# Kernel optimization log

Measured on AMD Instinct MI355X. Metric: run time of the kernel, lower is better.

Reference implementation:

```python
import jax, jax.numpy as jnp
import numpy as np

TRUNCATE = 4.0
SIGMA_MIN, SIGMA_MAX, NUM_STEPS = 0.5, 20.0, 200
RADIUS = int(TRUNCATE * SIGMA_MAX + 0.5)  # 80
KSIZE = 2 * RADIUS + 1                    # 161
B, C, H, W = 64, 3, 512, 512


def setup_inputs() -> dict:
    key = jax.random.key(0)
    k1, k2 = jax.random.split(key)
    x = jax.random.normal(k1, (B, C, H, W), dtype=jnp.float32)
    # geometric sigma schedule, as used in inverse-heat-dissipation models
    blur_sigmas = jnp.exp(
        jnp.linspace(np.log(SIGMA_MIN), np.log(SIGMA_MAX), NUM_STEPS)
    ).astype(jnp.float32)
    fwd_steps = jax.random.randint(k2, (B,), 0, NUM_STEPS, dtype=jnp.int32)
    return {"x": x, "blur_sigmas": blur_sigmas, "fwd_steps": fwd_steps}


def _gaussian_kernels_1d(sigmas, dtype):
    # torchvision formula: normalized exp(-0.5*(t/sigma)^2) on linspace(-half, half, K)
    half = (KSIZE - 1) / 2.0
    t = jnp.linspace(-half, half, KSIZE, dtype=dtype)        # [K]
    pdf = jnp.exp(-0.5 * (t[None, :] / sigmas[:, None]) ** 2)  # [B, K]
    return pdf / pdf.sum(axis=1, keepdims=True)


def reference(x, blur_sigmas, fwd_steps):
    b, c, h, w = x.shape
    sig = blur_sigmas[fwd_steps] + 1e-6                      # [B] per-sample sigma
    k1d = _gaussian_kernels_1d(sig, x.dtype)                 # [B, K]
    kc = jnp.repeat(k1d, c, axis=0)                          # [B*C, K] depthwise

    pad = KSIZE // 2
    xp = jnp.pad(x, ((0, 0), (0, 0), (pad, pad), (pad, pad)), mode="reflect")
    lhs = xp.reshape(1, b * c, h + 2 * pad, w + 2 * pad)

    dn_shape = (1, b * c, 1, 1)  # placeholder rhs shape for dim numbers
    dn = jax.lax.conv_dimension_numbers(lhs.shape, (b * c, 1, KSIZE, 1),
                                        ("NCHW", "OIHW", "NCHW"))
    # vertical pass: [1, BC, H+2p, W+2p] -> [1, BC, H, W+2p]
    y = jax.lax.conv_general_dilated(
        lhs, kc.reshape(b * c, 1, KSIZE, 1), (1, 1), "VALID",
        dimension_numbers=dn, feature_group_count=b * c)
    # horizontal pass: -> [1, BC, H, W]
    y = jax.lax.conv_general_dilated(
        y, kc.reshape(b * c, 1, 1, KSIZE), (1, 1), "VALID",
        dimension_numbers=dn, feature_group_count=b * c)
    return y.reshape(b, c, h, w)
```

## Files before the change

### kernel.cpp

```cpp
#include <hip/hip_runtime.h>
#include <hip/hip_fp16.h>


#define B_   64
#define C_   3
#define H_   512
#define W_   512
#define RMAX 80
#define NW   224
#define WOFF 112
#define RROW 288
#define SROW 64

typedef float    f32x16 __attribute__((ext_vector_type(16)));
typedef _Float16 f16x8  __attribute__((ext_vector_type(8)));

__device__ __forceinline__ int refl(int g) {
    int a = g < 0 ? -g : g;
    int c = 1022 - a;
    return a < c ? a : c;
}

__global__ __launch_bounds__(256) void k_weights(const float* __restrict__ sig,
                                                 const int* __restrict__ steps,
                                                 int* __restrict__ rad,
                                                 unsigned int* __restrict__ gw2) {
    const int b = blockIdx.x;
    const float sigma = sig[steps[b]] + 1e-6f;
    const int t = (int)threadIdx.x;
    const int d = t - 128;
    float e = 0.f;
    if (d >= -RMAX && d <= RMAX) {
        const float u = (float)d / sigma;
        e = expf(-0.5f * u * u);
    }
    __shared__ float red[256];
    __shared__ float wv[256];
    red[t] = e;
    __syncthreads();
    for (int s = 128; s > 0; s >>= 1) {
        if (t < s) red[t] += red[t + s];
        __syncthreads();
    }
    const float inv = 1.0f / red[0];
    int r = (int)ceilf(6.0f * sigma);
    if (r > RMAX) r = RMAX;
    if (r < 1)    r = 1;
    wv[t] = (d >= -r && d <= r) ? e * inv : 0.f;
    __syncthreads();
    if (t < NW) {
        const __half h0 = __float2half(wv[t + 16]);
        const __half h1 = __float2half(wv[t + 17]);
        gw2[b * NW + t] = (unsigned int)__half_as_ushort(h0) |
                          ((unsigned int)__half_as_ushort(h1) << 16);
    }
    if (t == 0) rad[b] = r;
}

__global__ __launch_bounds__(256, 4) void k_pass1(const float* __restrict__ x,
                                                  const unsigned int* __restrict__ gw2,
                                                  const int* __restrict__ rad,
                                                  __half* __restrict__ tmp) {
    __shared__ __align__(16) unsigned short sh[SROW * RROW];
    __shared__ unsigned int w2v[NW];
    const int tid = threadIdx.x;
    const int bid = blockIdx.x;
    const int bc  = bid >> 5;
    const int rem = bid & 31;
    const int y0  = (rem >> 3) << 7;
    const int x0  = (rem & 7) << 6;
    const int b   = bc / C_;
    const size_t img = (size_t)bc * (H_ * (size_t)W_);

    const int r  = rad[b];
    const int rp = (r + 7) & ~7;
    const int ns = (r + rp + 32 + 15) >> 4;
    const int Rr = 96 + 16 * ns;
    const int ystart = y0 - rp;

    if (tid < NW) w2v[tid] = gw2[b * NW + tid];

    {
        const int p0 = tid & 15;
        const int x4 = tid >> 4;
        const float* gsrc = x + img + (size_t)(x0 + x4 * 4);
        const int i7 = (2 * p0) & 7;
        for (int pr = p0; 2 * pr < Rr; pr += 16) {
            const int i0 = 2 * pr;
            const int gy0 = refl(ystart + i0);
            const int gy1 = refl(ystart + i0 + 1);
            const float4 va = *(const float4*)(gsrc + (size_t)gy0 * W_);
            const float4 vb = *(const float4*)(gsrc + (size_t)gy1 * W_);
            const int c = i0 >> 3;
            #pragma unroll
            for (int q = 0; q < 4; ++q) {
                const int xq = x4 * 4 + q;
                const int hidx = xq * RROW + ((c ^ (xq & 3)) << 3) + i7;
                const float fa = q == 0 ? va.x : q == 1 ? va.y : q == 2 ? va.z : va.w;
                const float fb = q == 0 ? vb.x : q == 1 ? vb.y : q == 2 ? vb.z : vb.w;
                *(__half2*)(sh + hidx) = __floats2half2_rn(fa, fb);
            }
        }
    }
    __syncthreads();

    const int l   = tid & 63;
    const int tau = tid >> 6;
    const int m   = l & 31;
    const int g   = l >> 5;
    const int ebase = WOFF + 8 * g - rp - m;
    const int cb0 = 4 * tau + g;
    const int key = m & 3;
    const int bb0 = m * RROW;
    const int bb1 = (32 + m) * RROW;

    f32x16 acc0 = {};
    f32x16 acc1 = {};
    for (int s = 0; s < ns; ++s) {
        const int e = ebase + 16 * s;
        union { unsigned int u[4]; f16x8 h; } A;
        A.u[0] = w2v[e];     A.u[1] = w2v[e + 2];
        A.u[2] = w2v[e + 4]; A.u[3] = w2v[e + 6];
        const int ph = ((cb0 + 2 * s) ^ key) << 3;
        const f16x8 bf0 = *(const f16x8*)(sh + bb0 + ph);
        const f16x8 bf1 = *(const f16x8*)(sh + bb1 + ph);
        acc0 = __builtin_amdgcn_mfma_f32_32x32x16_f16(A.h, bf0, acc0, 0, 0, 0);
        acc1 = __builtin_amdgcn_mfma_f32_32x32x16_f16(A.h, bf1, acc1, 0, 0, 0);
    }

    __half* tb = tmp + img + (size_t)(y0 + 32 * tau) * W_ + x0 + m;
    #pragma unroll
    for (int reg = 0; reg < 16; ++reg) {
        const int row = (reg & 3) + 8 * (reg >> 2) + 4 * g;
        tb[(size_t)row * W_]      = __float2half(acc0[reg]);
        tb[(size_t)row * W_ + 32] = __float2half(acc1[reg]);
    }
}

__global__ __launch_bounds__(256, 4) void k_pass2(const __half* __restrict__ tmp,
                                                  const unsigned int* __restrict__ gw2,
                                                  const int* __restrict__ rad,
                                                  float* __restrict__ out) {
    __shared__ __align__(16) unsigned short sh[SROW * RROW];
    __shared__ unsigned int w2v[NW];
    const int tid = threadIdx.x;
    const int bid = blockIdx.x;
    const int bc  = bid >> 5;
    const int rem = bid & 31;
    const int y0  = (rem >> 2) << 6;
    const int x0  = (rem & 3) << 7;
    const int b   = bc / C_;
    const size_t img = (size_t)bc * (H_ * (size_t)W_);

    const int r   = rad[b];
    const int rp  = (r + 7) & ~7;
    const int ns  = (r + rp + 32 + 15) >> 4;
    const int NC  = 12 + 2 * ns;
    const int i0g = x0 - rp;

    if (tid < NW) w2v[tid] = gw2[b * NW + tid];

    {
        const int row  = tid >> 2;
        const int cq   = tid & 3;
        const __half* grow = tmp + img + (size_t)(y0 + row) * W_;
        const int rkey = row & 3;
        for (int c = cq; c < NC; c += 4) {
            const int gi = i0g + c * 8;
            const int hidx = row * RROW + ((c ^ rkey) << 3);
            if (gi >= 0 && gi + 8 <= W_) {
                *(int4*)(sh + hidx) = *(const int4*)(grow + gi);
            } else {
                #pragma unroll
                for (int j = 0; j < 8; ++j)
                    sh[hidx + j] = __half_as_ushort(grow[refl(gi + j)]);
            }
        }
    }
    __syncthreads();

    const int l   = tid & 63;
    const int w   = tid >> 6;
    const int m   = l & 31;
    const int g   = l >> 5;
    const int tau = w >> 1;
    const int nup = (w & 1) * 2;
    const int ebase = WOFF + 8 * g - rp - m;
    const int arow  = 32 * tau + m;
    const int abase = arow * RROW;
    const int akey  = arow & 3;
    const int ca0   = 4 * nup + g;

    f32x16 acc0 = {};
    f32x16 acc1 = {};
    for (int s = 0; s < ns; ++s) {
        const int e = ebase + 16 * s;
        union { unsigned int u[4]; f16x8 h; } Wf;
        Wf.u[0] = w2v[e];     Wf.u[1] = w2v[e + 2];
        Wf.u[2] = w2v[e + 4]; Wf.u[3] = w2v[e + 6];
        const int c = ca0 + 2 * s;
        const f16x8 af0 = *(const f16x8*)(sh + abase + ((c ^ akey) << 3));
        const f16x8 af1 = *(const f16x8*)(sh + abase + (((c + 4) ^ akey) << 3));
        acc0 = __builtin_amdgcn_mfma_f32_32x32x16_f16(af0, Wf.h, acc0, 0, 0, 0);
        acc1 = __builtin_amdgcn_mfma_f32_32x32x16_f16(af1, Wf.h, acc1, 0, 0, 0);
    }

    float* ob = out + img + (size_t)(y0 + 32 * tau) * W_ + x0 + 32 * nup + m;
    #pragma unroll
    for (int reg = 0; reg < 16; ++reg) {
        const int row = (reg & 3) + 8 * (reg >> 2) + 4 * g;
        ob[(size_t)row * W_]      = acc0[reg];
        ob[(size_t)row * W_ + 32] = acc1[reg];
    }
}

extern "C" void kernel_launch(void* const* d_in, const int* in_sizes, int n_in,
                              void* d_out, int out_size, void* d_ws, size_t ws_size,
                              hipStream_t stream) {
    const float* x     = (const float*)d_in[0];
    const float* sig   = (const float*)d_in[1];
    const int*   steps = (const int*)d_in[2];
    float* out = (float*)d_out;

    char* ws = (char*)d_ws;
    int*          rad = (int*)ws;
    unsigned int* gw2 = (unsigned int*)(ws + 1024);
    __half*       tmp = (__half*)(ws + 65536);

    k_weights<<<B_, 256, 0, stream>>>(sig, steps, rad, gw2);
    k_pass1<<<B_ * C_ * 32, 256, 0, stream>>>(x, gw2, rad, tmp);
    k_pass2<<<B_ * C_ * 32, 256, 0, stream>>>(tmp, gw2, rad, out);
}
```

Before: 420.1 us.

## Fuse weight generation into passes and enlarge tiles for more halo reuse

Removes the separate weight kernel: each block of both passes now builds the Gaussian weights itself in shared memory. Pass 1 tiles grow to 256 rows by 64 columns with four accumulators per wave, and the block index is remapped so blocks of the same image run close together. Pass 2 now loads full 512-wide rows and fills the reflected halo inside shared memory instead of branching on global loads. The aim is to cut halo re-reads and one launch. The cost is redundant weight computation per block, more shared memory and fewer blocks, which may reduce occupancy.

New measurement: 398.3 us. 5.2% less time.

```diff
diff --git a/kernel.cpp b/kernel.cpp
--- a/kernel.cpp
+++ b/kernel.cpp
@@ -9,8 +9,8 @@
 #define RMAX 80
 #define NW   224
 #define WOFF 112
-#define RROW 288
-#define SROW 64
+#define RROW1 416
+#define IW2   672
 
 typedef float    f32x16 __attribute__((ext_vector_type(16)));
 typedef _Float16 f16x8  __attribute__((ext_vector_type(8)));
@@ -21,64 +21,59 @@
     return a < c ? a : c;
 }
 
-__global__ __launch_bounds__(256) void k_weights(const float* __restrict__ sig,
-                                                 const int* __restrict__ steps,
-                                                 int* __restrict__ rad,
-                                                 unsigned int* __restrict__ gw2) {
-    const int b = blockIdx.x;
-    const float sigma = sig[steps[b]] + 1e-6f;
-    const int t = (int)threadIdx.x;
-    const int d = t - 128;
+__device__ __forceinline__ int make_weights(float sigma, float* scr, float* red,
+                                            unsigned int* w2v, int tid) {
+    const int d = tid - 128;
     float e = 0.f;
     if (d >= -RMAX && d <= RMAX) {
         const float u = (float)d / sigma;
         e = expf(-0.5f * u * u);
     }
-    __shared__ float red[256];
-    __shared__ float wv[256];
-    red[t] = e;
+    scr[tid] = e;
+    red[tid] = e;
     __syncthreads();
     for (int s = 128; s > 0; s >>= 1) {
-        if (t < s) red[t] += red[t + s];
+        if (tid < s) red[tid] += red[tid + s];
         __syncthreads();
     }
     const float inv = 1.0f / red[0];
     int r = (int)ceilf(6.0f * sigma);
     if (r > RMAX) r = RMAX;
     if (r < 1)    r = 1;
-    wv[t] = (d >= -r && d <= r) ? e * inv : 0.f;
-    __syncthreads();
-    if (t < NW) {
-        const __half h0 = __float2half(wv[t + 16]);
-        const __half h1 = __float2half(wv[t + 17]);
-        gw2[b * NW + t] = (unsigned int)__half_as_ushort(h0) |
-                          ((unsigned int)__half_as_ushort(h1) << 16);
-    }
-    if (t == 0) rad[b] = r;
-}
-
-__global__ __launch_bounds__(256, 4) void k_pass1(const float* __restrict__ x,
-                                                  const unsigned int* __restrict__ gw2,
-                                                  const int* __restrict__ rad,
-                                                  __half* __restrict__ tmp) {
-    __shared__ __align__(16) unsigned short sh[SROW * RROW];
+    if (tid < NW) {
+        const int d0 = tid - 112;
+        const float w0 = (d0     >= -r && d0     <= r) ? scr[tid + 16] * inv : 0.f;
+        const float w1 = (d0 + 1 >= -r && d0 + 1 <= r) ? scr[tid + 17] * inv : 0.f;
+        w2v[tid] = (unsigned int)__half_as_ushort(__float2half(w0)) |
+                   ((unsigned int)__half_as_ushort(__float2half(w1)) << 16);
+    }
+    __syncthreads();
+    return r;
+}
+
+__global__ __launch_bounds__(256) void k_pass1(const float* __restrict__ x,
+                                               const float* __restrict__ sig,
+                                               const int* __restrict__ steps,
+                                               __half* __restrict__ tmp) {
+    __shared__ __align__(16) unsigned short sh[64 * RROW1];
     __shared__ unsigned int w2v[NW];
     const int tid = threadIdx.x;
-    const int bid = blockIdx.x;
-    const int bc  = bid >> 5;
-    const int rem = bid & 31;
-    const int y0  = (rem >> 3) << 7;
+    int bid = blockIdx.x;
+    bid = ((bid & 7) * 384) + (bid >> 3);
+    const int bc  = bid >> 4;
+    const int rem = bid & 15;
+    const int y0  = (rem >> 3) << 8;
     const int x0  = (rem & 7) << 6;
     const int b   = bc / C_;
     const size_t img = (size_t)bc * (H_ * (size_t)W_);
 
-    const int r  = rad[b];
+    const float sigma = sig[steps[b]] + 1e-6f;
+    float* scr = (float*)sh;
+    const int r  = make_weights(sigma, scr, scr + 256, w2v, tid);
     const int rp = (r + 7) & ~7;
-    const int ns = (r + rp + 32 + 15) >> 4;
-    const int Rr = 96 + 16 * ns;
+    const int ns = (r + rp + 47) >> 4;
+    const int Rr = 224 + 16 * ns;
     const int ystart = y0 - rp;
-
-    if (tid < NW) w2v[tid] = gw2[b * NW + tid];
 
     {
         const int p0 = tid & 15;
@@ -86,131 +81,146 @@
         const float* gsrc = x + img + (size_t)(x0 + x4 * 4);
         const int i7 = (2 * p0) & 7;
         for (int pr = p0; 2 * pr < Rr; pr += 16) {
-            const int i0 = 2 * pr;
+            const int i0  = 2 * pr;
             const int gy0 = refl(ystart + i0);
             const int gy1 = refl(ystart + i0 + 1);
             const float4 va = *(const float4*)(gsrc + (size_t)gy0 * W_);
             const float4 vb = *(const float4*)(gsrc + (size_t)gy1 * W_);
+            const float* fa = (const float*)&va;
+            const float* fb = (const float*)&vb;
             const int c = i0 >> 3;
             #pragma unroll
             for (int q = 0; q < 4; ++q) {
                 const int xq = x4 * 4 + q;
-                const int hidx = xq * RROW + ((c ^ (xq & 3)) << 3) + i7;
-                const float fa = q == 0 ? va.x : q == 1 ? va.y : q == 2 ? va.z : va.w;
-                const float fb = q == 0 ? vb.x : q == 1 ? vb.y : q == 2 ? vb.z : vb.w;
-                *(__half2*)(sh + hidx) = __floats2half2_rn(fa, fb);
+                const int hidx = xq * RROW1 + ((c ^ (xq & 3)) << 3) + i7;
+                *(__half2*)(sh + hidx) = __floats2half2_rn(fa[q], fb[q]);
             }
         }
     }
     __syncthreads();
 
     const int l   = tid & 63;
-    const int tau = tid >> 6;
+    const int wv_ = tid >> 6;
     const int m   = l & 31;
     const int g   = l >> 5;
+    const int key = m & 3;
     const int ebase = WOFF + 8 * g - rp - m;
-    const int cb0 = 4 * tau + g;
-    const int key = m & 3;
-    const int bb0 = m * RROW;
-    const int bb1 = (32 + m) * RROW;
-
-    f32x16 acc0 = {};
-    f32x16 acc1 = {};
+    const int cA  = 4 * wv_ + g;
+    const int cB  = 4 * (wv_ + 4) + g;
+    const unsigned short* shm0 = sh + m * RROW1;
+    const unsigned short* shm1 = sh + (32 + m) * RROW1;
+
+    f32x16 a0 = {}, a1 = {}, a2 = {}, a3 = {};
     for (int s = 0; s < ns; ++s) {
         const int e = ebase + 16 * s;
         union { unsigned int u[4]; f16x8 h; } A;
         A.u[0] = w2v[e];     A.u[1] = w2v[e + 2];
         A.u[2] = w2v[e + 4]; A.u[3] = w2v[e + 6];
-        const int ph = ((cb0 + 2 * s) ^ key) << 3;
-        const f16x8 bf0 = *(const f16x8*)(sh + bb0 + ph);
-        const f16x8 bf1 = *(const f16x8*)(sh + bb1 + ph);
-        acc0 = __builtin_amdgcn_mfma_f32_32x32x16_f16(A.h, bf0, acc0, 0, 0, 0);
-        acc1 = __builtin_amdgcn_mfma_f32_32x32x16_f16(A.h, bf1, acc1, 0, 0, 0);
-    }
-
-    __half* tb = tmp + img + (size_t)(y0 + 32 * tau) * W_ + x0 + m;
+        const int phA = ((cA + 2 * s) ^ key) << 3;
+        const int phB = ((cB + 2 * s) ^ key) << 3;
+        const f16x8 b00 = *(const f16x8*)(shm0 + phA);
+        const f16x8 b01 = *(const f16x8*)(shm1 + phA);
+        const f16x8 b10 = *(const f16x8*)(shm0 + phB);
+        const f16x8 b11 = *(const f16x8*)(shm1 + phB);
+        a0 = __builtin_amdgcn_mfma_f32_32x32x16_f16(A.h, b00, a0, 0, 0, 0);
+        a1 = __builtin_amdgcn_mfma_f32_32x32x16_f16(A.h, b01, a1, 0, 0, 0);
+        a2 = __builtin_amdgcn_mfma_f32_32x32x16_f16(A.h, b10, a2, 0, 0, 0);
+        a3 = __builtin_amdgcn_mfma_f32_32x32x16_f16(A.h, b11, a3, 0, 0, 0);
+    }
+
+    __half* tb0 = tmp + img + (size_t)(y0 + 32 * wv_) * W_ + x0 + m;
+    __half* tb1 = tmp + img + (size_t)(y0 + 32 * (wv_ + 4)) * W_ + x0 + m;
     #pragma unroll
     for (int reg = 0; reg < 16; ++reg) {
         const int row = (reg & 3) + 8 * (reg >> 2) + 4 * g;
-        tb[(size_t)row * W_]      = __float2half(acc0[reg]);
-        tb[(size_t)row * W_ + 32] = __float2half(acc1[reg]);
-    }
-}
-
-__global__ __launch_bounds__(256, 4) void k_pass2(const __half* __restrict__ tmp,
-                                                  const unsigned int* __restrict__ gw2,
-                                                  const int* __restrict__ rad,
-                                                  float* __restrict__ out) {
-    __shared__ __align__(16) unsigned short sh[SROW * RROW];
+        tb0[(size_t)row * W_]      = __float2half(a0[reg]);
+        tb0[(size_t)row * W_ + 32] = __float2half(a1[reg]);
+        tb1[(size_t)row * W_]      = __float2half(a2[reg]);
+        tb1[(size_t)row * W_ + 32] = __float2half(a3[reg]);
+    }
+}
+
+__global__ __launch_bounds__(256) void k_pass2(const __half* __restrict__ tmp,
+                                               const float* __restrict__ sig,
+                                               const int* __restrict__ steps,
+                                               float* __restrict__ out) {
+    __shared__ __align__(16) unsigned short sh[32 * IW2];
     __shared__ unsigned int w2v[NW];
     const int tid = threadIdx.x;
     const int bid = blockIdx.x;
-    const int bc  = bid >> 5;
-    const int rem = bid & 31;
-    const int y0  = (rem >> 2) << 6;
-    const int x0  = (rem & 3) << 7;
+    const int bc  = bid >> 4;
+    const int y0  = (bid & 15) << 5;
     const int b   = bc / C_;
     const size_t img = (size_t)bc * (H_ * (size_t)W_);
 
-    const int r   = rad[b];
-    const int rp  = (r + 7) & ~7;
-    const int ns  = (r + rp + 32 + 15) >> 4;
-    const int NC  = 12 + 2 * ns;
-    const int i0g = x0 - rp;
-
-    if (tid < NW) w2v[tid] = gw2[b * NW + tid];
-
+    const float sigma = sig[steps[b]] + 1e-6f;
+    float* scr = (float*)sh;
+    const int r  = make_weights(sigma, scr, scr + 256, w2v, tid);
+    const int rp = (r + 7) & ~7;
+    const int ns = (r + rp + 47) >> 4;
+
+    const int row  = tid >> 3;
+    const int cq   = tid & 7;
+    const int rkey = row & 3;
     {
-        const int row  = tid >> 2;
-        const int cq   = tid & 3;
         const __half* grow = tmp + img + (size_t)(y0 + row) * W_;
-        const int rkey = row & 3;
-        for (int c = cq; c < NC; c += 4) {
-            const int gi = i0g + c * 8;
-            const int hidx = row * RROW + ((c ^ rkey) << 3);
-            if (gi >= 0 && gi + 8 <= W_) {
-                *(int4*)(sh + hidx) = *(const int4*)(grow + gi);
-            } else {
-                #pragma unroll
-                for (int j = 0; j < 8; ++j)
-                    sh[hidx + j] = __half_as_ushort(grow[refl(gi + j)]);
-            }
+        const int cb = rp >> 3;
+        for (int k = cq; k < 64; k += 8) {
+            const int c = cb + k;
+            *(int4*)(sh + row * IW2 + ((c ^ rkey) << 3)) =
+                *(const int4*)(grow + k * 8);
         }
     }
     __syncthreads();
+    {
+        const int nh = 16 * ns - 32;
+        const int rbase = row * IW2;
+        for (int e = cq; e < nh; e += 8) {
+            const int ip = e < rp ? e : e + 512;
+            const int gx = ip - rp;
+            const int is = refl(gx) + rp;
+            const unsigned short v =
+                sh[rbase + (((is >> 3) ^ rkey) << 3) + (is & 7)];
+            sh[rbase + (((ip >> 3) ^ rkey) << 3) + (ip & 7)] = v;
+        }
+    }
+    __syncthreads();
 
     const int l   = tid & 63;
-    const int w   = tid >> 6;
+    const int wv_ = tid >> 6;
     const int m   = l & 31;
     const int g   = l >> 5;
-    const int tau = w >> 1;
-    const int nup = (w & 1) * 2;
+    const int akey  = m & 3;
     const int ebase = WOFF + 8 * g - rp - m;
-    const int arow  = 32 * tau + m;
-    const int abase = arow * RROW;
-    const int akey  = arow & 3;
-    const int ca0   = 4 * nup + g;
-
-    f32x16 acc0 = {};
-    f32x16 acc1 = {};
+    const unsigned short* shm = sh + m * IW2;
+    const int c0 = 16 * wv_ + g;
+
+    f32x16 a0 = {}, a1 = {}, a2 = {}, a3 = {};
     for (int s = 0; s < ns; ++s) {
         const int e = ebase + 16 * s;
         union { unsigned int u[4]; f16x8 h; } Wf;
         Wf.u[0] = w2v[e];     Wf.u[1] = w2v[e + 2];
         Wf.u[2] = w2v[e + 4]; Wf.u[3] = w2v[e + 6];
-        const int c = ca0 + 2 * s;
-        const f16x8 af0 = *(const f16x8*)(sh + abase + ((c ^ akey) << 3));
-        const f16x8 af1 = *(const f16x8*)(sh + abase + (((c + 4) ^ akey) << 3));
-        acc0 = __builtin_amdgcn_mfma_f32_32x32x16_f16(af0, Wf.h, acc0, 0, 0, 0);
-        acc1 = __builtin_amdgcn_mfma_f32_32x32x16_f16(af1, Wf.h, acc1, 0, 0, 0);
-    }
-
-    float* ob = out + img + (size_t)(y0 + 32 * tau) * W_ + x0 + 32 * nup + m;
+        const int cs = c0 + 2 * s;
+        const f16x8 f0 = *(const f16x8*)(shm + (((cs     ) ^ akey) << 3));
+        const f16x8 f1 = *(const f16x8*)(shm + (((cs +  4) ^ akey) << 3));
+        const f16x8 f2 = *(const f16x8*)(shm + (((cs +  8) ^ akey) << 3));
+        const f16x8 f3 = *(const f16x8*)(shm + (((cs + 12) ^ akey) << 3));
+        a0 = __builtin_amdgcn_mfma_f32_32x32x16_f16(f0, Wf.h, a0, 0, 0, 0);
+        a1 = __builtin_amdgcn_mfma_f32_32x32x16_f16(f1, Wf.h, a1, 0, 0, 0);
+        a2 = __builtin_amdgcn_mfma_f32_32x32x16_f16(f2, Wf.h, a2, 0, 0, 0);
+        a3 = __builtin_amdgcn_mfma_f32_32x32x16_f16(f3, Wf.h, a3, 0, 0, 0);
+    }
+
+    float* ob = out + img + (size_t)y0 * W_ + 128 * wv_ + m;
     #pragma unroll
     for (int reg = 0; reg < 16; ++reg) {
-        const int row = (reg & 3) + 8 * (reg >> 2) + 4 * g;
-        ob[(size_t)row * W_]      = acc0[reg];
-        ob[(size_t)row * W_ + 32] = acc1[reg];
+        const int orow = (reg & 3) + 8 * (reg >> 2) + 4 * g;
+        float* orp_ = ob + (size_t)orow * W_;
+        orp_[0]  = a0[reg];
+        orp_[32] = a1[reg];
+        orp_[64] = a2[reg];
+        orp_[96] = a3[reg];
     }
 }
 
@@ -221,13 +231,8 @@
     const float* sig   = (const float*)d_in[1];
     const int*   steps = (const int*)d_in[2];
     float* out = (float*)d_out;
-
-    char* ws = (char*)d_ws;
-    int*          rad = (int*)ws;
-    unsigned int* gw2 = (unsigned int*)(ws + 1024);
-    __half*       tmp = (__half*)(ws + 65536);
-
-    k_weights<<<B_, 256, 0, stream>>>(sig, steps, rad, gw2);
-    k_pass1<<<B_ * C_ * 32, 256, 0, stream>>>(x, gw2, rad, tmp);
-    k_pass2<<<B_ * C_ * 32, 256, 0, stream>>>(tmp, gw2, rad, out);
-}
+    __half* tmp = (__half*)d_ws;
+
+    k_pass1<<<B_ * C_ * 16, 256, 0, stream>>>(x, sig, steps, tmp);
+    k_pass2<<<B_ * C_ * 16, 256, 0, stream>>>(tmp, sig, steps, out);
+}
```
